# Kernel tuning notes

Measured on AMD Instinct MI355X. Metric: run time of the kernel, lower is better.

Reference implementation:

```python
import jax, jax.numpy as jnp
import numpy as np

D_MODEL = 1024
NUM_HEADS = 16
D_HEAD = D_MODEL // NUM_HEADS


def rotate_half(x):
    half = x.shape[-1] // 2
    x1, x2 = x[..., :half], x[..., half:]
    return jnp.concatenate((-x2, x1), axis=-1)


def rope_cos_sin(seq_len, d_head, dtype):
    # inv_freq over even dims of d_head
    inv_freq = 1.0 / (10000.0 ** (jnp.arange(0, d_head, 2, dtype=jnp.float32) / d_head))
    t = jnp.arange(seq_len, dtype=jnp.float32)
    freqs = jnp.einsum('i,j->ij', t, inv_freq)        # [L, d_head/2]
    emb = jnp.concatenate((freqs, freqs), axis=-1)    # [L, d_head]
    return jnp.cos(emb).astype(dtype), jnp.sin(emb).astype(dtype)


def setup_inputs() -> dict:
    key = jax.random.key(0)
    ks = jax.random.split(key, 9)
    B, L = 2, 2048
    s = 1.0 / np.sqrt(D_MODEL)
    return {
        'x': jax.random.normal(ks[0], (B, L, D_MODEL), dtype=jnp.float32),
        'Wq': jax.random.normal(ks[1], (D_MODEL, D_MODEL), dtype=jnp.float32) * s,
        'bq': jax.random.normal(ks[2], (D_MODEL,), dtype=jnp.float32) * 0.02,
        'Wk': jax.random.normal(ks[3], (D_MODEL, D_MODEL), dtype=jnp.float32) * s,
        'bk': jax.random.normal(ks[4], (D_MODEL,), dtype=jnp.float32) * 0.02,
        'Wv': jax.random.normal(ks[5], (D_MODEL, D_MODEL), dtype=jnp.float32) * s,
        'bv': jax.random.normal(ks[6], (D_MODEL,), dtype=jnp.float32) * 0.02,
        'Wo': jax.random.normal(ks[7], (D_MODEL, D_MODEL), dtype=jnp.float32) * s,
        'bo': jax.random.normal(ks[8], (D_MODEL,), dtype=jnp.float32) * 0.02,
    }


def reference(x, Wq, bq, Wk, bk, Wv, bv, Wo, bo):
    B, L, D = x.shape
    H, Dh = NUM_HEADS, D_HEAD
    scale = Dh ** -0.5

    # projections: torch Linear is x @ W.T + b; here W stored as [in, out]-like
    # square matrices, so treat Wq etc. directly as x @ Wq + bq.
    q = (x @ Wq + bq).reshape(B, L, H, Dh).transpose(0, 2, 1, 3)  # [B,H,L,Dh]
    k = (x @ Wk + bk).reshape(B, L, H, Dh).transpose(0, 2, 1, 3)
    v = (x @ Wv + bv).reshape(B, L, H, Dh).transpose(0, 2, 1, 3)

    cos, sin = rope_cos_sin(L, Dh, x.dtype)  # [L, Dh]
    cos = cos[None, None]  # [1,1,L,Dh]
    sin = sin[None, None]
    q = q * cos + rotate_half(q) * sin
    k = k * cos + rotate_half(k) * sin

    attn = jnp.einsum('bhqd,bhkd->bhqk', q, k) * scale  # [B,H,L,L]
    attn = jax.nn.softmax(attn, axis=-1)
    out = jnp.einsum('bhqk,bhkd->bhqd', attn, v)        # [B,H,L,Dh]
    out = out.transpose(0, 2, 1, 3).reshape(B, L, D)
    return out @ Wo + bo
```

## Files before the change

### kernel.cpp

```cpp
#include <hip/hip_runtime.h>
#include <cmath>

#define D_MODEL  1024
#define NHEADS   16
#define DHEAD    64
#define BATCH    2
#define SEQ      2048
#define MROWS    (BATCH * SEQ)
#define HALF_DH  32
#define BHTOT    (BATCH * NHEADS)
#define QROWS    (BHTOT * SEQ)

#define SCQ (0.125f * 1.44269504088896340736f)

typedef __attribute__((ext_vector_type(8))) short short8;
typedef __attribute__((ext_vector_type(4))) float f32x4;
typedef __attribute__((ext_vector_type(16))) float f32x16;

#define MFMA16(A,B,C) __builtin_amdgcn_mfma_f32_16x16x32_bf16(A,B,C,0,0,0)
#define MFMA32(A,B,C) __builtin_amdgcn_mfma_f32_32x32x16_bf16(A,B,C,0,0,0)

__device__ __forceinline__ unsigned short f2bf(float f) {
    unsigned int u = __float_as_uint(f);
    u += 0x7fffu + ((u >> 16) & 1u);
    return (unsigned short)(u >> 16);
}

__device__ __forceinline__ void gload_lds16(const void* g, void* l) {
    __builtin_amdgcn_global_load_lds(
        (const __attribute__((address_space(1))) unsigned int*)g,
        (__attribute__((address_space(3))) unsigned int*)l,
        16, 0, 0);
}

__global__ __launch_bounds__(256)
void prep_kernel(const float* __restrict__ x,
                 const float* __restrict__ Wq, const float* __restrict__ Wk,
                 const float* __restrict__ Wv, const float* __restrict__ Wo,
                 unsigned short* __restrict__ xb,
                 unsigned short* __restrict__ wqT, unsigned short* __restrict__ wkT,
                 unsigned short* __restrict__ wvT, unsigned short* __restrict__ woT,
                 float* __restrict__ cosT, float* __restrict__ sinT)
{
    __shared__ unsigned short T[64][68];
    const int bid = blockIdx.x;
    const int tid = threadIdx.x;

    if (bid < 4096) {
        int i = bid * 256 + tid;
        float4 v = ((const float4*)x)[i];
        ushort4 o;
        o.x = f2bf(v.x); o.y = f2bf(v.y); o.z = f2bf(v.z); o.w = f2bf(v.w);
        ((ushort4*)xb)[i] = o;
    } else if (bid < 5120) {
        int b2 = bid - 4096;
        int z  = b2 >> 8;
        int bx = (b2 & 255) >> 4;
        int by = b2 & 15;
        const float* W; unsigned short* Wt;
        switch (z) {
            case 0:  W = Wq; Wt = wqT; break;
            case 1:  W = Wk; Wt = wkT; break;
            case 2:  W = Wv; Wt = wvT; break;
            default: W = Wo; Wt = woT; break;
        }
        const int k0 = bx * 64, n0 = by * 64;
        const int r = tid >> 4, cq = tid & 15;
        #pragma unroll
        for (int p = 0; p < 4; ++p) {
            int kk = r + 16 * p;
            float4 vv = *(const float4*)&W[(size_t)(k0 + kk) * D_MODEL + n0 + cq * 4];
            T[cq * 4 + 0][kk] = f2bf(vv.x);
            T[cq * 4 + 1][kk] = f2bf(vv.y);
            T[cq * 4 + 2][kk] = f2bf(vv.z);
            T[cq * 4 + 3][kk] = f2bf(vv.w);
        }
        __syncthreads();
        #pragma unroll
        for (int p = 0; p < 4; ++p) {
            int n = r + 16 * p;
            ushort4 ov;
            ov.x = T[n][cq * 4 + 0]; ov.y = T[n][cq * 4 + 1];
            ov.z = T[n][cq * 4 + 2]; ov.w = T[n][cq * 4 + 3];
            *(ushort4*)&Wt[(size_t)(n0 + n) * D_MODEL + k0 + cq * 4] = ov;
        }
    } else {
        int idx = (bid - 5120) * 256 + tid;
        int l = idx >> 5;
        int j = idx & 31;
        float inv = powf(10000.0f, -(float)(2 * j) / (float)DHEAD);
        float ang = (float)l * inv;
        cosT[idx] = cosf(ang);
        sinT[idx] = sinf(ang);
    }
}

__global__ __launch_bounds__(256)
void qkv_proj_kernel(const unsigned short* __restrict__ A,
                     const unsigned short* __restrict__ wqT, const unsigned short* __restrict__ wkT,
                     const unsigned short* __restrict__ wvT,
                     const float* __restrict__ bq, const float* __restrict__ bk,
                     const float* __restrict__ bv,
                     const float* __restrict__ cosT, const float* __restrict__ sinT,
                     unsigned short* __restrict__ qb, unsigned short* __restrict__ kb,
                     unsigned short* __restrict__ vtb)
{
    __shared__ unsigned short SMEM[128 * 64 + 64 * 64];
    unsigned short* As = SMEM;
    unsigned short* Bs = SMEM + 128 * 64;

    const int z = blockIdx.z;
    const unsigned short* Bt = (z == 0) ? wqT : (z == 1) ? wkT : wvT;
    const float* bias = (z == 0) ? bq : (z == 1) ? bk : bv;

    const int tid = threadIdx.x;
    const int w = tid >> 6, ln = tid & 63;
    const int c = ln & 15, g = ln >> 4;
    const int bm = blockIdx.x * 128, bn = blockIdx.y * 64;
    const int srow = ln >> 3, sblk = ln & 7;

    f32x4 acc[2][4];
    #pragma unroll
    for (int mi = 0; mi < 2; ++mi)
        #pragma unroll
        for (int ni = 0; ni < 4; ++ni) acc[mi][ni] = (f32x4){0.f, 0.f, 0.f, 0.f};

    for (int k0 = 0; k0 < D_MODEL; k0 += 64) {
        __syncthreads();
        #pragma unroll
        for (int i = 0; i < 4; ++i) {
            int chunk = w * 4 + i;
            int row = chunk * 8 + srow;
            int gcol = (sblk ^ (row & 7)) * 8;
            gload_lds16(&A[(size_t)(bm + row) * D_MODEL + k0 + gcol], &As[chunk * 512]);
        }
        #pragma unroll
        for (int i = 0; i < 2; ++i) {
            int chunk = w * 2 + i;
            int row = chunk * 8 + srow;
            int gcol = (sblk ^ (row & 7)) * 8;
            gload_lds16(&Bt[(size_t)(bn + row) * D_MODEL + k0 + gcol], &Bs[chunk * 512]);
        }
        __syncthreads();

        #pragma unroll
        for (int ks = 0; ks < 2; ++ks) {
            const int koff = (ks * 32 + g * 8) ^ ((c & 7) * 8);
            short8 af[2];
            #pragma unroll
            for (int mi = 0; mi < 2; ++mi)
                af[mi] = *(const short8*)&As[(w * 32 + mi * 16 + c) * 64 + koff];
            #pragma unroll
            for (int ni = 0; ni < 4; ++ni) {
                short8 bfr = *(const short8*)&Bs[(ni * 16 + c) * 64 + koff];
                #pragma unroll
                for (int mi = 0; mi < 2; ++mi)
                    acc[mi][ni] = MFMA16(af[mi], bfr, acc[mi][ni]);
            }
        }
    }

    float bv4[4];
    #pragma unroll
    for (int ni = 0; ni < 4; ++ni) bv4[ni] = bias[bn + ni * 16 + c];

    if (z < 2) {
        unsigned short* op = z ? kb : qb;
        const float qscale = (z == 0) ? SCQ : 1.0f;
        const int hy = blockIdx.y;
        #pragma unroll
        for (int mi = 0; mi < 2; ++mi) {
            #pragma unroll
            for (int r = 0; r < 4; ++r) {
                const int m = bm + w * 32 + mi * 16 + g * 4 + r;
                const int b = m >> 11, ll = m & (SEQ - 1);
                float v[4];
                #pragma unroll
                for (int ni = 0; ni < 4; ++ni) v[ni] = acc[mi][ni][r] + bv4[ni];
                #pragma unroll
                for (int ni = 0; ni < 2; ++ni) {
                    int d = ni * 16 + c;
                    float co = cosT[ll * HALF_DH + d];
                    float si = sinT[ll * HALF_DH + d];
                    float lo = v[ni], hi = v[ni + 2];
                    v[ni]     = lo * co - hi * si;
                    v[ni + 2] = hi * co + lo * si;
                }
                unsigned short* dst = op + ((size_t)(b * NHEADS + hy) * SEQ + ll) * DHEAD;
                #pragma unroll
                for (int ni = 0; ni < 4; ++ni) dst[ni * 16 + c] = f2bf(v[ni] * qscale);
            }
        }
    } else {
        unsigned short (*T)[136] = (unsigned short(*)[136])SMEM;
        __syncthreads();
        #pragma unroll
        for (int mi = 0; mi < 2; ++mi)
            #pragma unroll
            for (int r = 0; r < 4; ++r)
                #pragma unroll
                for (int ni = 0; ni < 4; ++ni)
                    T[ni * 16 + c][w * 32 + mi * 16 + g * 4 + r] = f2bf(acc[mi][ni][r] + bv4[ni]);
        __syncthreads();
        const int b  = bm >> 11;
        const int l0 = bm & (SEQ - 1);
        const int bh = b * NHEADS + blockIdx.y;
        unsigned short* Vo = vtb + (size_t)bh * DHEAD * SEQ;
        #pragma unroll
        for (int it = 0; it < 4; ++it) {
            int row  = (tid >> 4) + it * 16;
            int col8 = tid & 15;
            uint4 val = *(const uint4*)&T[row][col8 * 8];
            *(uint4*)&Vo[(size_t)row * SEQ + l0 + col8 * 8] = val;
        }
    }
}

__global__ __launch_bounds__(256)
void outproj_kernel(const unsigned short* __restrict__ A, const unsigned short* __restrict__ Bt,
                    const float* __restrict__ bias, float* __restrict__ out)
{
    __shared__ unsigned short As[128 * 64];
    __shared__ unsigned short Bs[64 * 64];
    const int tid = threadIdx.x;
    const int w = tid >> 6, ln = tid & 63;
    const int c = ln & 15, g = ln >> 4;
    const int bm = blockIdx.x * 128, bn = blockIdx.y * 64;
    const int srow = ln >> 3, sblk = ln & 7;

    f32x4 acc[2][4];
    #pragma unroll
    for (int mi = 0; mi < 2; ++mi)
        #pragma unroll
        for (int ni = 0; ni < 4; ++ni) acc[mi][ni] = (f32x4){0.f, 0.f, 0.f, 0.f};

    for (int k0 = 0; k0 < D_MODEL; k0 += 64) {
        __syncthreads();
        #pragma unroll
        for (int i = 0; i < 4; ++i) {
            int chunk = w * 4 + i;
            int row = chunk * 8 + srow;
            int gcol = (sblk ^ (row & 7)) * 8;
            gload_lds16(&A[(size_t)(bm + row) * D_MODEL + k0 + gcol], &As[chunk * 512]);
        }
        #pragma unroll
        for (int i = 0; i < 2; ++i) {
            int chunk = w * 2 + i;
            int row = chunk * 8 + srow;
            int gcol = (sblk ^ (row & 7)) * 8;
            gload_lds16(&Bt[(size_t)(bn + row) * D_MODEL + k0 + gcol], &Bs[chunk * 512]);
        }
        __syncthreads();

        #pragma unroll
        for (int ks = 0; ks < 2; ++ks) {
            const int koff = (ks * 32 + g * 8) ^ ((c & 7) * 8);
            short8 af[2];
            #pragma unroll
            for (int mi = 0; mi < 2; ++mi)
                af[mi] = *(const short8*)&As[(w * 32 + mi * 16 + c) * 64 + koff];
            #pragma unroll
            for (int ni = 0; ni < 4; ++ni) {
                short8 bfr = *(const short8*)&Bs[(ni * 16 + c) * 64 + koff];
                #pragma unroll
                for (int mi = 0; mi < 2; ++mi)
                    acc[mi][ni] = MFMA16(af[mi], bfr, acc[mi][ni]);
            }
        }
    }

    float bv4[4];
    #pragma unroll
    for (int ni = 0; ni < 4; ++ni) bv4[ni] = bias[bn + ni * 16 + c];
    #pragma unroll
    for (int mi = 0; mi < 2; ++mi)
        #pragma unroll
        for (int r = 0; r < 4; ++r) {
            const int m = bm + w * 32 + mi * 16 + g * 4 + r;
            #pragma unroll
            for (int ni = 0; ni < 4; ++ni)
                out[(size_t)m * D_MODEL + bn + ni * 16 + c] = acc[mi][ni][r] + bv4[ni];
        }
}

__global__ __launch_bounds__(256, 4)
void attn_mfma32_kernel(const unsigned short* __restrict__ Q, const unsigned short* __restrict__ K,
                        const unsigned short* __restrict__ Vt, unsigned short* __restrict__ O,
                        float* __restrict__ accP, float* __restrict__ ml, int nsplit)
{
    __shared__ unsigned short Ks[2][64 * 64];
    __shared__ unsigned short Vs[2][64 * 64];
    const int tid = threadIdx.x;
    const int w = tid >> 6, ln = tid & 63;
    const int ql = ln & 31;
    const int h  = ln >> 5;
    const int bh = blockIdx.y;
    const int q  = blockIdx.x * 128 + w * 32 + ql;
    const int split = blockIdx.z;
    const int ntile = SEQ / (64 * nsplit);
    const int kt0 = split * (SEQ / nsplit);
    const int srow = ln >> 3, sblk = ln & 7;

    const unsigned short* Qb = Q  + (size_t)bh * SEQ * DHEAD;
    const unsigned short* Kb = K  + (size_t)bh * SEQ * DHEAD;
    const unsigned short* Vb = Vt + (size_t)bh * DHEAD * SEQ;

    short8 qf[4];
    #pragma unroll
    for (int dk = 0; dk < 4; ++dk)
        qf[dk] = *(const short8*)&Qb[(size_t)q * DHEAD + dk * 16 + h * 8];

    short8 onesF;
    #pragma unroll
    for (int i = 0; i < 8; ++i) onesF[i] = (short)0x3F80;

    int offk[4];
    #pragma unroll
    for (int t = 0; t < 4; ++t) offk[t] = ((2 * t + h) ^ (ql & 7)) * 8;
    const int rA = ql * 64, rB = (32 + ql) * 64;

    f32x16 accO0, accO1, accS;
    #pragma unroll
    for (int r = 0; r < 16; ++r) { accO0[r] = 0.f; accO1[r] = 0.f; accS[r] = 0.f; }
    float mst = -1e30f;

    #pragma unroll
    for (int i = 0; i < 2; ++i) {
        int chunk = w * 2 + i;
        int row = chunk * 8 + srow;
        int gcol = (sblk ^ (row & 7)) * 8;
        gload_lds16(&Kb[(size_t)(kt0 + row) * DHEAD + gcol], &Ks[0][chunk * 512]);
        gload_lds16(&Vb[(size_t)row * SEQ + kt0 + gcol],     &Vs[0][chunk * 512]);
    }
    __syncthreads();

    int cur = 0;
    for (int it = 0; it < ntile; ++it) {
        const int kt = kt0 + it * 64;
        if (it + 1 < ntile) {
            #pragma unroll
            for (int i = 0; i < 2; ++i) {
                int chunk = w * 2 + i;
                int row = chunk * 8 + srow;
                int gcol = (sblk ^ (row & 7)) * 8;
                gload_lds16(&Kb[(size_t)(kt + 64 + row) * DHEAD + gcol], &Ks[cur ^ 1][chunk * 512]);
                gload_lds16(&Vb[(size_t)row * SEQ + kt + 64 + gcol],     &Vs[cur ^ 1][chunk * 512]);
            }
        }

        f32x16 s0, s1;
        #pragma unroll
        for (int r = 0; r < 16; ++r) { s0[r] = 0.f; s1[r] = 0.f; }
        #pragma unroll
        for (int dk = 0; dk < 4; ++dk) {
            short8 kf0 = *(const short8*)&Ks[cur][rA + offk[dk]];
            short8 kf1 = *(const short8*)&Ks[cur][rB + offk[dk]];
            s0 = MFMA32(kf0, qf[dk], s0);
            s1 = MFMA32(kf1, qf[dk], s1);
        }

        float a0 = fmaxf(fmaxf(s0[0], s0[1]), s0[2]);
        float a1 = fmaxf(fmaxf(s0[3], s0[4]), s0[5]);
        float a2 = fmaxf(fmaxf(s0[6], s0[7]), s0[8]);
        float a3 = fmaxf(fmaxf(s0[9], s0[10]), s0[11]);
        float a4 = fmaxf(fmaxf(s0[12], s0[13]), s0[14]);
        float a5 = fmaxf(fmaxf(s0[15], s1[0]), s1[1]);
        float a6 = fmaxf(fmaxf(s1[2], s1[3]), s1[4]);
        float a7 = fmaxf(fmaxf(s1[5], s1[6]), s1[7]);
        float a8 = fmaxf(fmaxf(s1[8], s1[9]), s1[10]);
        float a9 = fmaxf(fmaxf(s1[11], s1[12]), s1[13]);
        float aA = fmaxf(s1[14], s1[15]);
        float b0 = fmaxf(fmaxf(a0, a1), a2);
        float b1 = fmaxf(fmaxf(a3, a4), a5);
        float b2 = fmaxf(fmaxf(a6, a7), a8);
        float b3 = fmaxf(a9, aA);
        float mx = fmaxf(fmaxf(fmaxf(b0, b1), b2), b3);
        mx = fmaxf(mx, __shfl_xor(mx, 32));

        if (!__all(mx - mst <= 4.0f)) {
            const float mn = fmaxf(mst, mx);
            const float rsc = exp2f(mst - mn);
            #pragma unroll
            for (int r = 0; r < 16; ++r) { accO0[r] *= rsc; accO1[r] *= rsc; }
            accS[0] *= rsc;
            mst = mn;
        }

        #pragma unroll
        for (int r = 0; r < 16; ++r) {
            s0[r] = exp2f(s0[r] - mst);
            s1[r] = exp2f(s1[r] - mst);
        }

        short8 pf[4];
        #define REPACK_T(T, SV)                                                          \
        {                                                                                \
            unsigned int wA0, wA1, wB0, wB1;                                             \
            asm("v_cvt_pk_bf16_f32 %0, %1, %2" : "=v"(wA0)                               \
                : "v"((SV)[8 * ((T) & 1) + 0]), "v"((SV)[8 * ((T) & 1) + 1]));           \
            asm("v_cvt_pk_bf16_f32 %0, %1, %2" : "=v"(wA1)                               \
                : "v"((SV)[8 * ((T) & 1) + 2]), "v"((SV)[8 * ((T) & 1) + 3]));           \
            asm("v_cvt_pk_bf16_f32 %0, %1, %2" : "=v"(wB0)                               \
                : "v"((SV)[8 * ((T) & 1) + 4]), "v"((SV)[8 * ((T) & 1) + 5]));           \
            asm("v_cvt_pk_bf16_f32 %0, %1, %2" : "=v"(wB1)                               \
                : "v"((SV)[8 * ((T) & 1) + 6]), "v"((SV)[8 * ((T) & 1) + 7]));           \
            asm("v_permlane32_swap_b32 %0, %1" : "+v"(wA0), "+v"(wB0));                  \
            asm("v_permlane32_swap_b32 %0, %1" : "+v"(wA1), "+v"(wB1));                  \
            union { short8 v; unsigned int u[4]; } tmp;                                  \
            tmp.u[0] = wA0; tmp.u[1] = wA1; tmp.u[2] = wB0; tmp.u[3] = wB1;              \
            pf[T] = tmp.v;                                                               \
        }
        REPACK_T(0, s0) REPACK_T(1, s0) REPACK_T(2, s1) REPACK_T(3, s1)
        #undef REPACK_T

        #pragma unroll
        for (int t = 0; t < 4; ++t) {
            short8 vf0 = *(const short8*)&Vs[cur][rA + offk[t]];
            short8 vf1 = *(const short8*)&Vs[cur][rB + offk[t]];
            accS  = MFMA32(onesF, pf[t], accS);
            accO0 = MFMA32(vf0, pf[t], accO0);
            accO1 = MFMA32(vf1, pf[t], accO1);
        }

        __syncthreads();
        cur ^= 1;
    }

    const float accL = accS[0];
    if (nsplit == 1) {
        const int b = bh >> 4, hh = bh & 15;
        const float inv = 1.0f / accL;
        unsigned short* dst = O + ((size_t)(b * SEQ + q)) * D_MODEL + hh * DHEAD;
        #define EPI(ACC, DC)                                                             \
        {                                                                                \
            _Pragma("unroll")                                                            \
            for (int rq = 0; rq < 4; ++rq) {                                             \
                float a0 = (ACC)[4 * rq + 0] * inv, a1 = (ACC)[4 * rq + 1] * inv;        \
                float a2 = (ACC)[4 * rq + 2] * inv, a3 = (ACC)[4 * rq + 3] * inv;        \
                unsigned int p0, p1;                                                     \
                asm("v_cvt_pk_bf16_f32 %0, %1, %2" : "=v"(p0) : "v"(a0), "v"(a1));       \
                asm("v_cvt_pk_bf16_f32 %0, %1, %2" : "=v"(p1) : "v"(a2), "v"(a3));       \
                uint2 pk; pk.x = p0; pk.y = p1;                                          \
                *(uint2*)(dst + 32 * (DC) + 8 * rq + 4 * h) = pk;                        \
            }                                                                            \
        }
        EPI(accO0, 0) EPI(accO1, 1)
        #undef EPI
    } else {
        float* base = accP + ((size_t)(split * BHTOT + bh) * SEQ + q) * 64;
        #pragma unroll
        for (int rq = 0; rq < 4; ++rq) {
            float4 v0, v1;
            v0.x = accO0[4 * rq + 0]; v0.y = accO0[4 * rq + 1];
            v0.z = accO0[4 * rq + 2]; v0.w = accO0[4 * rq + 3];
            v1.x = accO1[4 * rq + 0]; v1.y = accO1[4 * rq + 1];
            v1.z = accO1[4 * rq + 2]; v1.w = accO1[4 * rq + 3];
            *(float4*)&base[8 * rq + 4 * h]      = v0;
            *(float4*)&base[32 + 8 * rq + 4 * h] = v1;
        }
        if (h == 0) {
            float2 v; v.x = mst; v.y = accL;
            ((float2*)ml)[(size_t)(split * BHTOT + bh) * SEQ + q] = v;
        }
    }
}

__global__ __launch_bounds__(256)
void combine2_kernel(const float* __restrict__ accP, const float* __restrict__ ml,
                     unsigned short* __restrict__ ob)
{
    int t = blockIdx.x * 256 + threadIdx.x;
    int d4  = (t & 15) * 4;
    int bhq = t >> 4;
    const float2* ML = (const float2*)ml;
    float2 m0 = ML[bhq];
    float2 m1 = ML[(size_t)QROWS + bhq];
    float M  = fmaxf(m0.x, m1.x);
    float w0 = exp2f(m0.x - M);
    float w1 = exp2f(m1.x - M);
    float inv = 1.0f / (w0 * m0.y + w1 * m1.y);
    float4 a0 = *(const float4*)&accP[(size_t)bhq * 64 + d4];
    float4 a1 = *(const float4*)&accP[(size_t)QROWS * 64 + (size_t)bhq * 64 + d4];
    float o0 = (a0.x * w0 + a1.x * w1) * inv;
    float o1 = (a0.y * w0 + a1.y * w1) * inv;
    float o2 = (a0.z * w0 + a1.z * w1) * inv;
    float o3 = (a0.w * w0 + a1.w * w1) * inv;
    int bh = bhq >> 11, q = bhq & (SEQ - 1);
    int b = bh >> 4, hh = bh & 15;
    ushort4 ov;
    ov.x = f2bf(o0); ov.y = f2bf(o1); ov.z = f2bf(o2); ov.w = f2bf(o3);
    *(ushort4*)&ob[((size_t)(b * SEQ + q)) * D_MODEL + hh * DHEAD + d4] = ov;
}

extern "C" void kernel_launch(void* const* d_in, const int* in_sizes, int n_in,
                              void* d_out, int out_size, void* d_ws, size_t ws_size,
                              hipStream_t stream)
{
    const float* x  = (const float*)d_in[0];
    const float* Wq = (const float*)d_in[1];
    const float* bq = (const float*)d_in[2];
    const float* Wk = (const float*)d_in[3];
    const float* bk = (const float*)d_in[4];
    const float* Wv = (const float*)d_in[5];
    const float* bv = (const float*)d_in[6];
    const float* Wo = (const float*)d_in[7];
    const float* bo = (const float*)d_in[8];

    char* p = (char*)d_ws;
    float* cosT = (float*)p;            p += (size_t)SEQ * HALF_DH * 4;
    float* sinT = (float*)p;            p += (size_t)SEQ * HALF_DH * 4;
    unsigned short* xb  = (unsigned short*)p; p += (size_t)MROWS * D_MODEL * 2;
    unsigned short* wqT = (unsigned short*)p; p += (size_t)D_MODEL * D_MODEL * 2;
    unsigned short* wkT = (unsigned short*)p; p += (size_t)D_MODEL * D_MODEL * 2;
    unsigned short* wvT = (unsigned short*)p; p += (size_t)D_MODEL * D_MODEL * 2;
    unsigned short* woT = (unsigned short*)p; p += (size_t)D_MODEL * D_MODEL * 2;
    unsigned short* qb  = (unsigned short*)p; p += (size_t)MROWS * D_MODEL * 2;
    unsigned short* kb  = (unsigned short*)p; p += (size_t)MROWS * D_MODEL * 2;
    unsigned short* vtb = (unsigned short*)p; p += (size_t)MROWS * D_MODEL * 2;
    unsigned short* ob  = (unsigned short*)p; p += (size_t)MROWS * D_MODEL * 2;
    float* accP = (float*)p;            p += (size_t)2 * QROWS * 64 * 4;
    float* ml   = (float*)p;            p += (size_t)2 * QROWS * 2 * 4;
    size_t need2 = (size_t)(p - (char*)d_ws);
    const int nsplit = (ws_size >= need2) ? 2 : 1;

    prep_kernel<<<5376, 256, 0, stream>>>(x, Wq, Wk, Wv, Wo,
                                          xb, wqT, wkT, wvT, woT, cosT, sinT);

    qkv_proj_kernel<<<dim3(MROWS / 128, D_MODEL / 64, 3), 256, 0, stream>>>(
        xb, wqT, wkT, wvT, bq, bk, bv, cosT, sinT, qb, kb, vtb);

    attn_mfma32_kernel<<<dim3(SEQ / 128, BHTOT, nsplit), 256, 0, stream>>>(
        qb, kb, vtb, ob, accP, ml, nsplit);

    if (nsplit == 2)
        combine2_kernel<<<(QROWS * 16) / 256, 256, 0, stream>>>(accP, ml, ob);

    outproj_kernel<<<dim3(MROWS / 128, D_MODEL / 64), 256, 0, stream>>>(ob, woT, bo, (float*)d_out);
}
```

Before: 140.8 us.

## Stage K/V tiles through registers into padded LDS instead of direct global-to-LDS loads

Replaces the direct global_load_lds async copies of the K and V tiles with ordinary vector loads into registers. The registers are written to LDS mid-iteration, after the softmax exponentials. The XOR-swizzled layout is replaced by a row stride padded to 68 elements to avoid bank conflicts. This costs extra VGPRs and explicit LDS write instructions and may lower occupancy. It removes the swizzle index math and lets the global loads overlap with the QK and softmax compute.

```diff
diff --git a/kernel.cpp b/kernel.cpp
--- a/kernel.cpp
+++ b/kernel.cpp
@@ -10,6 +10,7 @@
 #define HALF_DH  32
 #define BHTOT    (BATCH * NHEADS)
 #define QROWS    (BHTOT * SEQ)
+#define LDK      68
 
 #define SCQ (0.125f * 1.44269504088896340736f)
 
@@ -288,8 +289,8 @@
                         const unsigned short* __restrict__ Vt, unsigned short* __restrict__ O,
                         float* __restrict__ accP, float* __restrict__ ml, int nsplit)
 {
-    __shared__ unsigned short Ks[2][64 * 64];
-    __shared__ unsigned short Vs[2][64 * 64];
+    __shared__ unsigned short Ks[2][64 * LDK];
+    __shared__ unsigned short Vs[2][64 * LDK];
     const int tid = threadIdx.x;
     const int w = tid >> 6, ln = tid & 63;
     const int ql = ln & 31;
@@ -299,7 +300,9 @@
     const int split = blockIdx.z;
     const int ntile = SEQ / (64 * nsplit);
     const int kt0 = split * (SEQ / nsplit);
-    const int srow = ln >> 3, sblk = ln & 7;
+
+    const int srow0 = 16 * w + (ln >> 3);
+    const int scol  = (ln & 7) * 8;
 
     const unsigned short* Qb = Q  + (size_t)bh * SEQ * DHEAD;
     const unsigned short* Kb = K  + (size_t)bh * SEQ * DHEAD;
@@ -314,23 +317,25 @@
     #pragma unroll
     for (int i = 0; i < 8; ++i) onesF[i] = (short)0x3F80;
 
-    int offk[4];
-    #pragma unroll
-    for (int t = 0; t < 4; ++t) offk[t] = ((2 * t + h) ^ (ql & 7)) * 8;
-    const int rA = ql * 64, rB = (32 + ql) * 64;
+    const int rA = ql * LDK, rB = (32 + ql) * LDK;
 
     f32x16 accO0, accO1, accS;
     #pragma unroll
     for (int r = 0; r < 16; ++r) { accO0[r] = 0.f; accO1[r] = 0.f; accS[r] = 0.f; }
     float mst = -1e30f;
 
+    short8 kreg[2], vreg[2];
     #pragma unroll
     for (int i = 0; i < 2; ++i) {
-        int chunk = w * 2 + i;
-        int row = chunk * 8 + srow;
-        int gcol = (sblk ^ (row & 7)) * 8;
-        gload_lds16(&Kb[(size_t)(kt0 + row) * DHEAD + gcol], &Ks[0][chunk * 512]);
-        gload_lds16(&Vb[(size_t)row * SEQ + kt0 + gcol],     &Vs[0][chunk * 512]);
+        int row = srow0 + 8 * i;
+        kreg[i] = *(const short8*)&Kb[(size_t)(kt0 + row) * DHEAD + scol];
+        vreg[i] = *(const short8*)&Vb[(size_t)row * SEQ + kt0 + scol];
+    }
+    #pragma unroll
+    for (int i = 0; i < 2; ++i) {
+        int row = srow0 + 8 * i;
+        *(short8*)&Ks[0][row * LDK + scol] = kreg[i];
+        *(short8*)&Vs[0][row * LDK + scol] = vreg[i];
     }
     __syncthreads();
 
@@ -340,11 +345,9 @@
         if (it + 1 < ntile) {
             #pragma unroll
             for (int i = 0; i < 2; ++i) {
-                int chunk = w * 2 + i;
-                int row = chunk * 8 + srow;
-                int gcol = (sblk ^ (row & 7)) * 8;
-                gload_lds16(&Kb[(size_t)(kt + 64 + row) * DHEAD + gcol], &Ks[cur ^ 1][chunk * 512]);
-                gload_lds16(&Vb[(size_t)row * SEQ + kt + 64 + gcol],     &Vs[cur ^ 1][chunk * 512]);
+                int row = srow0 + 8 * i;
+                kreg[i] = *(const short8*)&Kb[(size_t)(kt + 64 + row) * DHEAD + scol];
+                vreg[i] = *(const short8*)&Vb[(size_t)row * SEQ + kt + 64 + scol];
             }
         }
 
@@ -353,8 +356,8 @@
         for (int r = 0; r < 16; ++r) { s0[r] = 0.f; s1[r] = 0.f; }
         #pragma unroll
         for (int dk = 0; dk < 4; ++dk) {
-            short8 kf0 = *(const short8*)&Ks[cur][rA + offk[dk]];
-            short8 kf1 = *(const short8*)&Ks[cur][rB + offk[dk]];
+            short8 kf0 = *(const short8*)&Ks[cur][rA + (2 * dk + h) * 8];
+            short8 kf1 = *(const short8*)&Ks[cur][rB + (2 * dk + h) * 8];
             s0 = MFMA32(kf0, qf[dk], s0);
             s1 = MFMA32(kf1, qf[dk], s1);
         }
@@ -392,6 +395,15 @@
             s1[r] = exp2f(s1[r] - mst);
         }
 
+        if (it + 1 < ntile) {
+            #pragma unroll
+            for (int i = 0; i < 2; ++i) {
+                int row = srow0 + 8 * i;
+                *(short8*)&Ks[cur ^ 1][row * LDK + scol] = kreg[i];
+                *(short8*)&Vs[cur ^ 1][row * LDK + scol] = vreg[i];
+            }
+        }
+
         short8 pf[4];
         #define REPACK_T(T, SV)                                                          \
         {                                                                                \
@@ -415,8 +427,8 @@
 
         #pragma unroll
         for (int t = 0; t < 4; ++t) {
-            short8 vf0 = *(const short8*)&Vs[cur][rA + offk[t]];
-            short8 vf1 = *(const short8*)&Vs[cur][rB + offk[t]];
+            short8 vf0 = *(const short8*)&Vs[cur][rA + (2 * t + h) * 8];
+            short8 vf1 = *(const short8*)&Vs[cur][rB + (2 * t + h) * 8];
             accS  = MFMA32(onesF, pf[t], accS);
             accO0 = MFMA32(vf0, pf[t], accO0);
             accO1 = MFMA32(vf1, pf[t], accO1);
```

After: 151.4 us. +7.5%, slower.
